# Optimization experiments

Measured on AMD Instinct MI355X. Metric: run time of the kernel, lower is better.

Reference implementation:

```python
import jax, jax.numpy as jnp
import numpy as np

D_IN, H1, H2, F1 = 2048, 128, 64, 32


def setup_inputs() -> dict:
    key = jax.random.key(0)
    ks = jax.random.split(key, 13)
    s = lambda *sh: 1.0 / np.sqrt(sh[-1])
    return {
        "x": jax.random.normal(ks[0], (64, 512, D_IN), dtype=jnp.float32),
        "W_ih1": jax.random.uniform(ks[1], (H1, D_IN), jnp.float32, -s(H1), s(H1)),
        "W_hh1": jax.random.uniform(ks[2], (H1, H1), jnp.float32, -s(H1), s(H1)),
        "b_ih1": jax.random.uniform(ks[3], (H1,), jnp.float32, -s(H1), s(H1)),
        "b_hh1": jax.random.uniform(ks[4], (H1,), jnp.float32, -s(H1), s(H1)),
        "W_ih2": jax.random.uniform(ks[5], (H2, H1), jnp.float32, -s(H2), s(H2)),
        "W_hh2": jax.random.uniform(ks[6], (H2, H2), jnp.float32, -s(H2), s(H2)),
        "b_ih2": jax.random.uniform(ks[7], (H2,), jnp.float32, -s(H2), s(H2)),
        "b_hh2": jax.random.uniform(ks[8], (H2,), jnp.float32, -s(H2), s(H2)),
        "W_fc1": jax.random.uniform(ks[9], (F1, H2), jnp.float32, -s(F1), s(F1)),
        "b_fc1": jax.random.uniform(ks[10], (F1,), jnp.float32, -s(F1), s(F1)),
        "W_fc2": jax.random.uniform(ks[11], (1, F1), jnp.float32, -s(1), s(1)),
        "b_fc2": jax.random.uniform(ks[12], (1,), jnp.float32, -s(1), s(1)),
    }


def _rnn(x, W_ih, W_hh, b_ih, b_hh):
    # x: [B, T, D] -> outputs [B, T, H] (tanh RNN, h0 = 0)
    B = x.shape[0]
    H = W_hh.shape[0]
    # precompute the input projection once (big GEMM, outside the scan)
    xp = jnp.einsum('btd,hd->bth', x, W_ih) + b_ih  # [B, T, H]
    xp_t = jnp.swapaxes(xp, 0, 1)  # [T, B, H]

    def step(h, xpt):
        h_new = jnp.tanh(xpt + h @ W_hh.T + b_hh)
        return h_new, h_new

    h0 = jnp.zeros((B, H), dtype=x.dtype)
    _, ys = jax.lax.scan(step, h0, xp_t)  # ys: [T, B, H]
    return jnp.swapaxes(ys, 0, 1)


def reference(x, W_ih1, W_hh1, b_ih1, b_hh1, W_ih2, W_hh2, b_ih2, b_hh2,
              W_fc1, b_fc1, W_fc2, b_fc2):
    out1 = _rnn(x, W_ih1, W_hh1, b_ih1, b_hh1)      # [B, T, 128]
    # dropout is identity in eval mode
    out2 = _rnn(out1, W_ih2, W_hh2, b_ih2, b_hh2)   # [B, T, 64]
    h_last = out2[:, -1, :]                          # [B, 64]
    h = jax.nn.relu(h_last @ W_fc1.T + b_fc1)        # [B, 32]
    return h @ W_fc2.T + b_fc2                       # [B, 1]
```

## Files before the change

### kernel.cpp

```cpp
#include <hip/hip_runtime.h>

#define TT   512
#define DIN  2048
#define NH1  128
#define NH2  64
#define NB   64

typedef __attribute__((ext_vector_type(8))) __bf16 bf16x8;
typedef __attribute__((ext_vector_type(4))) float f32x4;

__device__ __forceinline__ float tanh_fast(float x) {
    x = fminf(fmaxf(x, -15.0f), 15.0f);
    float e = __expf(2.0f * x);
    return (e - 1.0f) / (e + 1.0f);
}

__device__ __forceinline__ float rlane(float v, int l) {
    return __int_as_float(__builtin_amdgcn_readlane(__float_as_int(v), l));
}

#define BAR() asm volatile("s_waitcnt lgkmcnt(0)\n\ts_barrier" ::: "memory")

__global__ __launch_bounds__(256, 1) void xp1_gemm(const float* __restrict__ x,
                                                   const float* __restrict__ W,
                                                   const float* __restrict__ bih1,
                                                   const float* __restrict__ bhh1,
                                                   float* __restrict__ xp1) {
    __shared__ __align__(16) __bf16 wl[2][NH1][40];

    const int tid  = threadIdx.x;
    const int lane = tid & 63;
    const int wv   = tid >> 6;
    const int quad = lane >> 4;
    const int l16  = lane & 15;
    const int m0   = blockIdx.x * 128 + wv * 32;

    const int wr = tid >> 1;
    const int wk = (tid & 1) * 16;

    float bias[8];
#pragma unroll
    for (int nt = 0; nt < 8; ++nt)
        bias[nt] = bih1[nt * 16 + l16] + bhh1[nt * 16 + l16];

    f32x4 acc[2][8];
#pragma unroll
    for (int ms = 0; ms < 2; ++ms)
#pragma unroll
        for (int nt = 0; nt < 8; ++nt)
            acc[ms][nt] = (f32x4){0.f, 0.f, 0.f, 0.f};

    const float* xr0 = x + (size_t)(m0 + l16) * DIN + quad * 8;
    const float* xr1 = x + (size_t)(m0 + 16 + l16) * DIN + quad * 8;
    const float* wp  = W + (size_t)wr * DIN + wk;

    float4 xa0 = *(const float4*)(xr0);
    float4 xb0 = *(const float4*)(xr0 + 4);
    float4 xa1 = *(const float4*)(xr1);
    float4 xb1 = *(const float4*)(xr1 + 4);
    float4 w0  = *(const float4*)(wp);
    float4 w1  = *(const float4*)(wp + 4);
    float4 w2  = *(const float4*)(wp + 8);
    float4 w3  = *(const float4*)(wp + 12);

    for (int kc = 0; kc < DIN; kc += 32) {
        {
            float wf[16] = {w0.x, w0.y, w0.z, w0.w, w1.x, w1.y, w1.z, w1.w,
                            w2.x, w2.y, w2.z, w2.w, w3.x, w3.y, w3.z, w3.w};
            bf16x8 hv0, lv0, hv1, lv1;
#pragma unroll
            for (int j = 0; j < 8; ++j) {
                __bf16 h = (__bf16)wf[j];
                hv0[j] = h;
                lv0[j] = (__bf16)(wf[j] - (float)h);
            }
#pragma unroll
            for (int j = 0; j < 8; ++j) {
                __bf16 h = (__bf16)wf[8 + j];
                hv1[j] = h;
                lv1[j] = (__bf16)(wf[8 + j] - (float)h);
            }
            *(bf16x8*)&wl[0][wr][wk]     = hv0;
            *(bf16x8*)&wl[0][wr][wk + 8] = hv1;
            *(bf16x8*)&wl[1][wr][wk]     = lv0;
            *(bf16x8*)&wl[1][wr][wk + 8] = lv1;
        }
        BAR();

        bf16x8 ah0, al0, ah1, al1;
        {
            float f0[8] = {xa0.x, xa0.y, xa0.z, xa0.w, xb0.x, xb0.y, xb0.z, xb0.w};
            float f1[8] = {xa1.x, xa1.y, xa1.z, xa1.w, xb1.x, xb1.y, xb1.z, xb1.w};
#pragma unroll
            for (int j = 0; j < 8; ++j) {
                __bf16 h0 = (__bf16)f0[j];
                ah0[j] = h0;
                al0[j] = (__bf16)(f0[j] - (float)h0);
                __bf16 h1 = (__bf16)f1[j];
                ah1[j] = h1;
                al1[j] = (__bf16)(f1[j] - (float)h1);
            }
        }

        if (kc + 32 < DIN) {
            xa0 = *(const float4*)(xr0 + kc + 32);
            xb0 = *(const float4*)(xr0 + kc + 36);
            xa1 = *(const float4*)(xr1 + kc + 32);
            xb1 = *(const float4*)(xr1 + kc + 36);
            w0  = *(const float4*)(wp + kc + 32);
            w1  = *(const float4*)(wp + kc + 36);
            w2  = *(const float4*)(wp + kc + 40);
            w3  = *(const float4*)(wp + kc + 44);
        }

#pragma unroll
        for (int nt = 0; nt < 8; ++nt) {
            bf16x8 bh = *(bf16x8*)&wl[0][nt * 16 + l16][quad * 8];
            bf16x8 bl = *(bf16x8*)&wl[1][nt * 16 + l16][quad * 8];
            acc[0][nt] = __builtin_amdgcn_mfma_f32_16x16x32_bf16(ah0, bh, acc[0][nt], 0, 0, 0);
            acc[0][nt] = __builtin_amdgcn_mfma_f32_16x16x32_bf16(al0, bh, acc[0][nt], 0, 0, 0);
            acc[0][nt] = __builtin_amdgcn_mfma_f32_16x16x32_bf16(ah0, bl, acc[0][nt], 0, 0, 0);
            acc[1][nt] = __builtin_amdgcn_mfma_f32_16x16x32_bf16(ah1, bh, acc[1][nt], 0, 0, 0);
            acc[1][nt] = __builtin_amdgcn_mfma_f32_16x16x32_bf16(al1, bh, acc[1][nt], 0, 0, 0);
            acc[1][nt] = __builtin_amdgcn_mfma_f32_16x16x32_bf16(ah1, bl, acc[1][nt], 0, 0, 0);
        }
        BAR();
    }

#pragma unroll
    for (int ms = 0; ms < 2; ++ms) {
        const int mb = m0 + ms * 16 + quad * 4;
#pragma unroll
        for (int nt = 0; nt < 8; ++nt) {
#pragma unroll
            for (int r = 0; r < 4; ++r)
                xp1[(size_t)(mb + r) * NH1 + nt * 16 + l16] = acc[ms][nt][r] + bias[nt];
        }
    }
}

__global__ __launch_bounds__(256, 1) void rnn_scan(
        const float* __restrict__ xp1,  const float* __restrict__ Whh1,
        const float* __restrict__ Wih2, const float* __restrict__ Whh2,
        const float* __restrict__ bih2, const float* __restrict__ bhh2,
        const float* __restrict__ Wfc1, const float* __restrict__ bfc1,
        const float* __restrict__ Wfc2, const float* __restrict__ bfc2,
        float* __restrict__ out) {
    __shared__ __align__(16) float h1buf[2][NH1];
    __shared__ __align__(16) float xp2buf[2][NH2];

    const int tid  = threadIdx.x;
    const int lane = tid & 63;
    const int wv   = tid >> 6;
    const int b    = blockIdx.x;

    const int kown = wv * 64;
    const int koth = 64 - kown;

    float wrow[128];
    float b2 = 0.0f;

    if (wv <= 1) {
        const int row = wv * 64 + lane;
        const float* src = Whh1 + (size_t)row * NH1;
#pragma unroll
        for (int i = 0; i < 128; i += 4) {
            float4 v = *(const float4*)&src[(kown + i) & 127];
            wrow[i] = v.x; wrow[i+1] = v.y; wrow[i+2] = v.z; wrow[i+3] = v.w;
        }
    } else if (wv == 2) {
        const float4* src = (const float4*)(Wih2 + (size_t)lane * NH1);
#pragma unroll
        for (int i = 0; i < 32; ++i) {
            float4 v = src[i];
            wrow[4*i+0] = v.x; wrow[4*i+1] = v.y;
            wrow[4*i+2] = v.z; wrow[4*i+3] = v.w;
        }
        b2 = bih2[lane] + bhh2[lane];
    } else {
        const float4* src = (const float4*)(Whh2 + (size_t)lane * NH2);
#pragma unroll
        for (int i = 0; i < 16; ++i) {
            float4 v = src[i];
            wrow[4*i+0] = v.x; wrow[4*i+1] = v.y;
            wrow[4*i+2] = v.z; wrow[4*i+3] = v.w;
        }
    }

    if (tid < 128) h1buf[0][tid] = 0.0f;

    const int row = wv * 64 + lane;
    const float* xprow = xp1 + ((size_t)b * TT) * NH1 + row;

    float xr[8], xrn[8];
    if (wv <= 1) {
#pragma unroll
        for (int j = 0; j < 8; ++j) xr[j] = xprow[(size_t)j * NH1];
    }

    __syncthreads();

    float hown   = 0.0f;
    float h2prev = 0.0f;

    for (int g = 0; g < 64; ++g) {
        if (wv <= 1 && g < 63) {
            const size_t t0 = (size_t)(g + 1) * 8;
#pragma unroll
            for (int j = 0; j < 8; ++j) xrn[j] = xprow[(t0 + j) * NH1];
        }
#pragma unroll
        for (int j = 0; j < 8; ++j) {
            const int s   = 8 * g + j + 1;
            const int cur = j & 1;
            const int nxt = cur ^ 1;
            if (wv <= 1) {
                float hoth = h1buf[cur][koth + lane];
                float a0 = xr[j], a1 = 0.f, a2 = 0.f, a3 = 0.f;
#pragma unroll
                for (int l = 0; l < 64; l += 4) {
                    a0 = fmaf(wrow[l],     rlane(hown, l),     a0);
                    a1 = fmaf(wrow[l + 1], rlane(hown, l + 1), a1);
                    a2 = fmaf(wrow[l + 2], rlane(hown, l + 2), a2);
                    a3 = fmaf(wrow[l + 3], rlane(hown, l + 3), a3);
                }
#pragma unroll
                for (int l = 0; l < 64; l += 4) {
                    a0 = fmaf(wrow[64 + l],     rlane(hoth, l),     a0);
                    a1 = fmaf(wrow[64 + l + 1], rlane(hoth, l + 1), a1);
                    a2 = fmaf(wrow[64 + l + 2], rlane(hoth, l + 2), a2);
                    a3 = fmaf(wrow[64 + l + 3], rlane(hoth, l + 3), a3);
                }
                float hv = tanh_fast((a0 + a1) + (a2 + a3));
                h1buf[nxt][row] = hv;
                hown = hv;
            } else if (wv == 2) {
                if (s >= 2) {
                    float2 hh = *(const float2*)&h1buf[cur][2 * lane];
                    float a0 = b2, a1 = 0.f, a2 = 0.f, a3 = 0.f;
#pragma unroll
                    for (int l = 0; l < 64; l += 2) {
                        float he0 = rlane(hh.x, l),     ho0 = rlane(hh.y, l);
                        float he1 = rlane(hh.x, l + 1), ho1 = rlane(hh.y, l + 1);
                        a0 = fmaf(wrow[2*l],     he0, a0);
                        a1 = fmaf(wrow[2*l + 1], ho0, a1);
                        a2 = fmaf(wrow[2*l + 2], he1, a2);
                        a3 = fmaf(wrow[2*l + 3], ho1, a3);
                    }
                    xp2buf[j & 1][lane] = (a0 + a1) + (a2 + a3);
                }
            } else {
                if (s >= 3) {
                    float xv = xp2buf[(j + 1) & 1][lane];
                    float a0 = 0.f, a1 = 0.f, a2 = 0.f, a3 = 0.f;
#pragma unroll
                    for (int l = 0; l < 64; l += 4) {
                        a0 = fmaf(wrow[l],     rlane(h2prev, l),     a0);
                        a1 = fmaf(wrow[l + 1], rlane(h2prev, l + 1), a1);
                        a2 = fmaf(wrow[l + 2], rlane(h2prev, l + 2), a2);
                        a3 = fmaf(wrow[l + 3], rlane(h2prev, l + 3), a3);
                    }
                    h2prev = tanh_fast(xv + ((a0 + a1) + (a2 + a3)));
                }
            }
            BAR();
        }
        if (wv <= 1 && g < 63) {
#pragma unroll
            for (int j = 0; j < 8; ++j) xr[j] = xrn[j];
        }
    }

    {
        if (wv == 2) {
            float2 hh = *(const float2*)&h1buf[0][2 * lane];
            float a0 = b2, a1 = 0.f, a2 = 0.f, a3 = 0.f;
#pragma unroll
            for (int l = 0; l < 64; l += 2) {
                float he0 = rlane(hh.x, l),     ho0 = rlane(hh.y, l);
                float he1 = rlane(hh.x, l + 1), ho1 = rlane(hh.y, l + 1);
                a0 = fmaf(wrow[2*l],     he0, a0);
                a1 = fmaf(wrow[2*l + 1], ho0, a1);
                a2 = fmaf(wrow[2*l + 2], he1, a2);
                a3 = fmaf(wrow[2*l + 3], ho1, a3);
            }
            xp2buf[0][lane] = (a0 + a1) + (a2 + a3);
        } else if (wv == 3) {
            float xv = xp2buf[1][lane];
            float a0 = 0.f, a1 = 0.f, a2 = 0.f, a3 = 0.f;
#pragma unroll
            for (int l = 0; l < 64; l += 4) {
                a0 = fmaf(wrow[l],     rlane(h2prev, l),     a0);
                a1 = fmaf(wrow[l + 1], rlane(h2prev, l + 1), a1);
                a2 = fmaf(wrow[l + 2], rlane(h2prev, l + 2), a2);
                a3 = fmaf(wrow[l + 3], rlane(h2prev, l + 3), a3);
            }
            h2prev = tanh_fast(xv + ((a0 + a1) + (a2 + a3)));
        }
        BAR();
    }
    if (wv == 3) {
        float xv = xp2buf[0][lane];
        float a0 = 0.f, a1 = 0.f, a2 = 0.f, a3 = 0.f;
#pragma unroll
        for (int l = 0; l < 64; l += 4) {
            a0 = fmaf(wrow[l],     rlane(h2prev, l),     a0);
            a1 = fmaf(wrow[l + 1], rlane(h2prev, l + 1), a1);
            a2 = fmaf(wrow[l + 2], rlane(h2prev, l + 2), a2);
            a3 = fmaf(wrow[l + 3], rlane(h2prev, l + 3), a3);
        }
        h2prev = tanh_fast(xv + ((a0 + a1) + (a2 + a3)));

        float wfc[64];
        const int fr = lane & 31;
        const float4* fsrc = (const float4*)(Wfc1 + (size_t)fr * NH2);
#pragma unroll
        for (int i = 0; i < 16; ++i) {
            float4 v = fsrc[i];
            wfc[4*i+0] = v.x; wfc[4*i+1] = v.y;
            wfc[4*i+2] = v.z; wfc[4*i+3] = v.w;
        }
        float a = (lane < 32) ? bfc1[lane] : 0.0f;
#pragma unroll
        for (int k = 0; k < 64; ++k)
            a = fmaf(wfc[k], rlane(h2prev, k), a);
        float v = (lane < 32) ? fmaxf(a, 0.0f) * Wfc2[lane] : 0.0f;
#pragma unroll
        for (int off = 16; off > 0; off >>= 1) v += __shfl_down(v, off);
        if (lane == 0) out[b] = v + bfc2[0];
    }
}

extern "C" void kernel_launch(void* const* d_in, const int* in_sizes, int n_in,
                              void* d_out, int out_size, void* d_ws, size_t ws_size,
                              hipStream_t stream) {
    const float* x     = (const float*)d_in[0];
    const float* Wih1  = (const float*)d_in[1];
    const float* Whh1  = (const float*)d_in[2];
    const float* bih1  = (const float*)d_in[3];
    const float* bhh1  = (const float*)d_in[4];
    const float* Wih2  = (const float*)d_in[5];
    const float* Whh2  = (const float*)d_in[6];
    const float* bih2  = (const float*)d_in[7];
    const float* bhh2  = (const float*)d_in[8];
    const float* Wfc1  = (const float*)d_in[9];
    const float* bfc1  = (const float*)d_in[10];
    const float* Wfc2  = (const float*)d_in[11];
    const float* bfc2  = (const float*)d_in[12];
    float* outp = (float*)d_out;

    float* xp1 = (float*)d_ws;

    xp1_gemm<<<dim3((NB * TT) / 128), dim3(256), 0, stream>>>(x, Wih1, bih1, bhh1, xp1);
    rnn_scan<<<dim3(NB), dim3(256), 0, stream>>>(xp1, Whh1, Wih2, Whh2, bih2, bhh2,
                                                 Wfc1, bfc1, Wfc2, bfc2, outp);
}
```

Baseline: 733.5 us.

## Replace readlane broadcasts with LDS float4 reads and packed FP32 FMA in RNN scan

In the recurrent scan, hidden-state values used to be broadcast across lanes with v_readlane. They are now read from shared memory as float4 broadcasts, and the matvecs use v_pk_fma_f32 on paired weights held in registers. Layer 2's hidden state moves from a register into a double-buffered LDS array so it can use the same pattern. The goal is to cut the per-step instruction count and the readlane latency on the serial critical path. The cost is extra LDS traffic and a different summation order.

Result: faster. 717.0 us (-2.2%).

```diff
diff --git a/kernel.cpp b/kernel.cpp
--- a/kernel.cpp
+++ b/kernel.cpp
@@ -8,6 +8,7 @@
 
 typedef __attribute__((ext_vector_type(8))) __bf16 bf16x8;
 typedef __attribute__((ext_vector_type(4))) float f32x4;
+typedef __attribute__((ext_vector_type(2))) float f32x2;
 
 __device__ __forceinline__ float tanh_fast(float x) {
     x = fminf(fmaxf(x, -15.0f), 15.0f);
@@ -17,6 +18,10 @@
 
 __device__ __forceinline__ float rlane(float v, int l) {
     return __int_as_float(__builtin_amdgcn_readlane(__float_as_int(v), l));
+}
+
+__device__ __forceinline__ void pkfma(f32x2& acc, f32x2 w, f32x2 h) {
+    asm("v_pk_fma_f32 %0, %1, %2, %0" : "+v"(acc) : "v"(w), "v"(h));
 }
 
 #define BAR() asm volatile("s_waitcnt lgkmcnt(0)\n\ts_barrier" ::: "memory")
@@ -148,33 +153,32 @@
         float* __restrict__ out) {
     __shared__ __align__(16) float h1buf[2][NH1];
     __shared__ __align__(16) float xp2buf[2][NH2];
+    __shared__ __align__(16) float h2buf[2][NH2];
 
     const int tid  = threadIdx.x;
     const int lane = tid & 63;
     const int wv   = tid >> 6;
     const int b    = blockIdx.x;
 
-    const int kown = wv * 64;
-    const int koth = 64 - kown;
-
-    float wrow[128];
+    f32x2 w2[64];
     float b2 = 0.0f;
 
     if (wv <= 1) {
         const int row = wv * 64 + lane;
-        const float* src = Whh1 + (size_t)row * NH1;
-#pragma unroll
-        for (int i = 0; i < 128; i += 4) {
-            float4 v = *(const float4*)&src[(kown + i) & 127];
-            wrow[i] = v.x; wrow[i+1] = v.y; wrow[i+2] = v.z; wrow[i+3] = v.w;
+        const float4* src = (const float4*)(Whh1 + (size_t)row * NH1);
+#pragma unroll
+        for (int i = 0; i < 32; ++i) {
+            float4 v = src[i];
+            w2[2 * i]     = (f32x2){v.x, v.y};
+            w2[2 * i + 1] = (f32x2){v.z, v.w};
         }
     } else if (wv == 2) {
         const float4* src = (const float4*)(Wih2 + (size_t)lane * NH1);
 #pragma unroll
         for (int i = 0; i < 32; ++i) {
             float4 v = src[i];
-            wrow[4*i+0] = v.x; wrow[4*i+1] = v.y;
-            wrow[4*i+2] = v.z; wrow[4*i+3] = v.w;
+            w2[2 * i]     = (f32x2){v.x, v.y};
+            w2[2 * i + 1] = (f32x2){v.z, v.w};
         }
         b2 = bih2[lane] + bhh2[lane];
     } else {
@@ -182,12 +186,13 @@
 #pragma unroll
         for (int i = 0; i < 16; ++i) {
             float4 v = src[i];
-            wrow[4*i+0] = v.x; wrow[4*i+1] = v.y;
-            wrow[4*i+2] = v.z; wrow[4*i+3] = v.w;
+            w2[2 * i]     = (f32x2){v.x, v.y};
+            w2[2 * i + 1] = (f32x2){v.z, v.w};
         }
     }
 
     if (tid < 128) h1buf[0][tid] = 0.0f;
+    if (tid < 64)  { h2buf[0][tid] = 0.0f; h2buf[1][tid] = 0.0f; }
 
     const int row = wv * 64 + lane;
     const float* xprow = xp1 + ((size_t)b * TT) * NH1 + row;
@@ -199,9 +204,6 @@
     }
 
     __syncthreads();
-
-    float hown   = 0.0f;
-    float h2prev = 0.0f;
 
     for (int g = 0; g < 64; ++g) {
         if (wv <= 1 && g < 63) {
@@ -215,52 +217,41 @@
             const int cur = j & 1;
             const int nxt = cur ^ 1;
             if (wv <= 1) {
-                float hoth = h1buf[cur][koth + lane];
-                float a0 = xr[j], a1 = 0.f, a2 = 0.f, a3 = 0.f;
-#pragma unroll
-                for (int l = 0; l < 64; l += 4) {
-                    a0 = fmaf(wrow[l],     rlane(hown, l),     a0);
-                    a1 = fmaf(wrow[l + 1], rlane(hown, l + 1), a1);
-                    a2 = fmaf(wrow[l + 2], rlane(hown, l + 2), a2);
-                    a3 = fmaf(wrow[l + 3], rlane(hown, l + 3), a3);
+                f32x2 aA = (f32x2){xr[j], 0.0f};
+                f32x2 aB = (f32x2){0.0f, 0.0f};
+#pragma unroll
+                for (int i = 0; i < 32; ++i) {
+                    float4 h4 = *(const float4*)&h1buf[cur][4 * i];
+                    pkfma(aA, w2[2 * i],     (f32x2){h4.x, h4.y});
+                    pkfma(aB, w2[2 * i + 1], (f32x2){h4.z, h4.w});
                 }
-#pragma unroll
-                for (int l = 0; l < 64; l += 4) {
-                    a0 = fmaf(wrow[64 + l],     rlane(hoth, l),     a0);
-                    a1 = fmaf(wrow[64 + l + 1], rlane(hoth, l + 1), a1);
-                    a2 = fmaf(wrow[64 + l + 2], rlane(hoth, l + 2), a2);
-                    a3 = fmaf(wrow[64 + l + 3], rlane(hoth, l + 3), a3);
-                }
-                float hv = tanh_fast((a0 + a1) + (a2 + a3));
+                float hv = tanh_fast((aA.x + aA.y) + (aB.x + aB.y));
                 h1buf[nxt][row] = hv;
-                hown = hv;
             } else if (wv == 2) {
                 if (s >= 2) {
-                    float2 hh = *(const float2*)&h1buf[cur][2 * lane];
-                    float a0 = b2, a1 = 0.f, a2 = 0.f, a3 = 0.f;
-#pragma unroll
-                    for (int l = 0; l < 64; l += 2) {
-                        float he0 = rlane(hh.x, l),     ho0 = rlane(hh.y, l);
-                        float he1 = rlane(hh.x, l + 1), ho1 = rlane(hh.y, l + 1);
-                        a0 = fmaf(wrow[2*l],     he0, a0);
-                        a1 = fmaf(wrow[2*l + 1], ho0, a1);
-                        a2 = fmaf(wrow[2*l + 2], he1, a2);
-                        a3 = fmaf(wrow[2*l + 3], ho1, a3);
+                    f32x2 aA = (f32x2){b2, 0.0f};
+                    f32x2 aB = (f32x2){0.0f, 0.0f};
+#pragma unroll
+                    for (int i = 0; i < 32; ++i) {
+                        float4 h4 = *(const float4*)&h1buf[cur][4 * i];
+                        pkfma(aA, w2[2 * i],     (f32x2){h4.x, h4.y});
+                        pkfma(aB, w2[2 * i + 1], (f32x2){h4.z, h4.w});
                     }
-                    xp2buf[j & 1][lane] = (a0 + a1) + (a2 + a3);
+                    xp2buf[j & 1][lane] = (aA.x + aA.y) + (aB.x + aB.y);
                 }
             } else {
                 if (s >= 3) {
                     float xv = xp2buf[(j + 1) & 1][lane];
-                    float a0 = 0.f, a1 = 0.f, a2 = 0.f, a3 = 0.f;
-#pragma unroll
-                    for (int l = 0; l < 64; l += 4) {
-                        a0 = fmaf(wrow[l],     rlane(h2prev, l),     a0);
-                        a1 = fmaf(wrow[l + 1], rlane(h2prev, l + 1), a1);
-                        a2 = fmaf(wrow[l + 2], rlane(h2prev, l + 2), a2);
-                        a3 = fmaf(wrow[l + 3], rlane(h2prev, l + 3), a3);
+                    f32x2 aA = (f32x2){0.0f, 0.0f};
+                    f32x2 aB = (f32x2){0.0f, 0.0f};
+#pragma unroll
+                    for (int i = 0; i < 16; ++i) {
+                        float4 h4 = *(const float4*)&h2buf[cur][4 * i];
+                        pkfma(aA, w2[2 * i],     (f32x2){h4.x, h4.y});
+                        pkfma(aB, w2[2 * i + 1], (f32x2){h4.z, h4.w});
                     }
-                    h2prev = tanh_fast(xv + ((a0 + a1) + (a2 + a3)));
+                    float h2v = tanh_fast(xv + ((aA.x + aA.y) + (aB.x + aB.y)));
+                    h2buf[nxt][lane] = h2v;
                 }
             }
             BAR();
@@ -273,43 +264,41 @@
 
     {
         if (wv == 2) {
-            float2 hh = *(const float2*)&h1buf[0][2 * lane];
-            float a0 = b2, a1 = 0.f, a2 = 0.f, a3 = 0.f;
-#pragma unroll
-            for (int l = 0; l < 64; l += 2) {
-                float he0 = rlane(hh.x, l),     ho0 = rlane(hh.y, l);
-                float he1 = rlane(hh.x, l + 1), ho1 = rlane(hh.y, l + 1);
-                a0 = fmaf(wrow[2*l],     he0, a0);
-                a1 = fmaf(wrow[2*l + 1], ho0, a1);
-                a2 = fmaf(wrow[2*l + 2], he1, a2);
-                a3 = fmaf(wrow[2*l + 3], ho1, a3);
-            }
-            xp2buf[0][lane] = (a0 + a1) + (a2 + a3);
+            f32x2 aA = (f32x2){b2, 0.0f};
+            f32x2 aB = (f32x2){0.0f, 0.0f};
+#pragma unroll
+            for (int i = 0; i < 32; ++i) {
+                float4 h4 = *(const float4*)&h1buf[0][4 * i];
+                pkfma(aA, w2[2 * i],     (f32x2){h4.x, h4.y});
+                pkfma(aB, w2[2 * i + 1], (f32x2){h4.z, h4.w});
+            }
+            xp2buf[0][lane] = (aA.x + aA.y) + (aB.x + aB.y);
         } else if (wv == 3) {
             float xv = xp2buf[1][lane];
-            float a0 = 0.f, a1 = 0.f, a2 = 0.f, a3 = 0.f;
-#pragma unroll
-            for (int l = 0; l < 64; l += 4) {
-                a0 = fmaf(wrow[l],     rlane(h2prev, l),     a0);
-                a1 = fmaf(wrow[l + 1], rlane(h2prev, l + 1), a1);
-                a2 = fmaf(wrow[l + 2], rlane(h2prev, l + 2), a2);
-                a3 = fmaf(wrow[l + 3], rlane(h2prev, l + 3), a3);
-            }
-            h2prev = tanh_fast(xv + ((a0 + a1) + (a2 + a3)));
+            f32x2 aA = (f32x2){0.0f, 0.0f};
+            f32x2 aB = (f32x2){0.0f, 0.0f};
+#pragma unroll
+            for (int i = 0; i < 16; ++i) {
+                float4 h4 = *(const float4*)&h2buf[0][4 * i];
+                pkfma(aA, w2[2 * i],     (f32x2){h4.x, h4.y});
+                pkfma(aB, w2[2 * i + 1], (f32x2){h4.z, h4.w});
+            }
+            float h2v = tanh_fast(xv + ((aA.x + aA.y) + (aB.x + aB.y)));
+            h2buf[1][lane] = h2v;
         }
         BAR();
     }
     if (wv == 3) {
         float xv = xp2buf[0][lane];
-        float a0 = 0.f, a1 = 0.f, a2 = 0.f, a3 = 0.f;
-#pragma unroll
-        for (int l = 0; l < 64; l += 4) {
-            a0 = fmaf(wrow[l],     rlane(h2prev, l),     a0);
-            a1 = fmaf(wrow[l + 1], rlane(h2prev, l + 1), a1);
-            a2 = fmaf(wrow[l + 2], rlane(h2prev, l + 2), a2);
-            a3 = fmaf(wrow[l + 3], rlane(h2prev, l + 3), a3);
-        }
-        h2prev = tanh_fast(xv + ((a0 + a1) + (a2 + a3)));
+        f32x2 aA = (f32x2){0.0f, 0.0f};
+        f32x2 aB = (f32x2){0.0f, 0.0f};
+#pragma unroll
+        for (int i = 0; i < 16; ++i) {
+            float4 h4 = *(const float4*)&h2buf[1][4 * i];
+            pkfma(aA, w2[2 * i],     (f32x2){h4.x, h4.y});
+            pkfma(aB, w2[2 * i + 1], (f32x2){h4.z, h4.w});
+        }
+        float h2last = tanh_fast(xv + ((aA.x + aA.y) + (aB.x + aB.y)));
 
         float wfc[64];
         const int fr = lane & 31;
@@ -323,7 +312,7 @@
         float a = (lane < 32) ? bfc1[lane] : 0.0f;
 #pragma unroll
         for (int k = 0; k < 64; ++k)
-            a = fmaf(wfc[k], rlane(h2prev, k), a);
+            a = fmaf(wfc[k], rlane(h2last, k), a);
         float v = (lane < 32) ? fmaxf(a, 0.0f) * Wfc2[lane] : 0.0f;
 #pragma unroll
         for (int off = 16; off > 0; off >>= 1) v += __shfl_down(v, off);
```
